# Optimization experiments

Measured on AMD Instinct MI355X. Metric: run time of the kernel, lower is better.

The kernel has to match this reference:

```python
import jax, jax.numpy as jnp
import numpy as np

B, T, I, H, O = 256, 512, 64, 512, 1


def _lstm_layer(x, Wih, Whh, bih, bhh):
    # x: [B, T, in]; Wih: [4H, in]; Whh: [4H, H]
    # Precompute input contribution for all timesteps (big GEMM, no recurrence).
    xg = jnp.einsum('bti,gi->btg', x, Wih) + bih + bhh  # [B, T, 4H]
    h0 = jnp.zeros((x.shape[0], Whh.shape[1]), x.dtype)
    c0 = jnp.zeros_like(h0)

    def step(carry, xt):
        h, c = carry
        gates = xt + h @ Whh.T  # [B, 4H]
        i, f, g, o = jnp.split(gates, 4, axis=-1)  # PyTorch gate order i,f,g,o
        i = jax.nn.sigmoid(i)
        f = jax.nn.sigmoid(f)
        g = jnp.tanh(g)
        o = jax.nn.sigmoid(o)
        c = f * c + i * g
        h = o * jnp.tanh(c)
        return (h, c), h

    _, hs = jax.lax.scan(step, (h0, c0), jnp.swapaxes(xg, 0, 1))  # [T, B, H]
    return jnp.swapaxes(hs, 0, 1)  # [B, T, H]


def setup_inputs() -> dict:
    key = jax.random.key(0)
    ks = jax.random.split(key, 12)
    s = 1.0 / np.sqrt(H)
    u = lambda k, shp: jax.random.uniform(k, shp, jnp.float32, -s, s)
    return {
        'x': jax.random.normal(ks[0], (B, T, I), jnp.float32),
        'Wih0': u(ks[1], (4 * H, I)),
        'Whh0': u(ks[2], (4 * H, H)),
        'bih0': u(ks[3], (4 * H,)),
        'bhh0': u(ks[4], (4 * H,)),
        'Wih1': u(ks[5], (4 * H, H)),
        'Whh1': u(ks[6], (4 * H, H)),
        'bih1': u(ks[7], (4 * H,)),
        'bhh1': u(ks[8], (4 * H,)),
        'Wfc': u(ks[9], (O, H)),
        'bfc': u(ks[10], (O,)),
    }


def reference(x, Wih0, Whh0, bih0, bhh0, Wih1, Whh1, bih1, bhh1, Wfc, bfc):
    h1 = _lstm_layer(x, Wih0, Whh0, bih0, bhh0)   # [B, T, H]
    h2 = _lstm_layer(h1, Wih1, Whh1, bih1, bhh1)  # [B, T, H]
    return h2[:, -1] @ Wfc.T + bfc  # [B, O]
```

## Files before the change

kernel.cpp:

```cpp
#include <hip/hip_runtime.h>

typedef unsigned short u16;
typedef unsigned long long u64;
typedef short bf16x8 __attribute__((ext_vector_type(8)));
typedef float f32x4 __attribute__((ext_vector_type(4)));

#define B_ 256
#define T_ 512
#define I_ 64
#define H_ 512
#define RING 32

#define OFF_F0    0u
#define OFF_F1    32768u
#define OFF_F2    65536u
#define OFF_F3    98304u
#define OFF_B0    131072u
#define OFF_B1    139264u
#define OFF_WIH0  147456u
#define OFF_WHH0  409600u
#define OFF_WIH1  2506752u
#define OFF_WHH1  4603904u
#define OFF_HX1   6701056u
#define OFF_H1R   7225344u
#define WS_NEEDED 15613952u

#define AQ __ATOMIC_RELAXED
#define SC __HIP_MEMORY_SCOPE_AGENT

static __device__ __forceinline__ u16 f2b(float f) {
  union { float f; unsigned u; } v; v.f = f;
  unsigned r = (v.u + 0x7FFFu + ((v.u >> 16) & 1u)) >> 16;
  return (u16)r;
}
static __device__ __forceinline__ float sigm(float x) { return 1.f / (1.f + __expf(-x)); }
static __device__ __forceinline__ float tanh_(float x) { return 1.f - 2.f / (__expf(2.f * x) + 1.f); }

static __device__ __forceinline__ void spin2(const unsigned* __restrict__ pa, unsigned tg) {
  unsigned a = __hip_atomic_load(pa, AQ, SC);
  for (;;) {
    unsigned b = __hip_atomic_load(pa, AQ, SC);
    if (!__any(a < tg)) break;
    a = __hip_atomic_load(pa, AQ, SC);
    if (!__any(b < tg)) break;
  }
}

__global__ void prep_kernel(const float* __restrict__ Wih0, const float* __restrict__ Whh0,
                            const float* __restrict__ bih0, const float* __restrict__ bhh0,
                            const float* __restrict__ Wih1, const float* __restrict__ Whh1,
                            const float* __restrict__ bih1, const float* __restrict__ bhh1,
                            const float* __restrict__ bfc, float* __restrict__ out,
                            char* __restrict__ ws) {
  unsigned* flags = (unsigned*)(ws + OFF_F0);
  float* b0 = (float*)(ws + OFF_B0);
  float* b1 = (float*)(ws + OFF_B1);
  u16* wih0b = (u16*)(ws + OFF_WIH0);
  u16* whh0b = (u16*)(ws + OFF_WHH0);
  u16* wih1b = (u16*)(ws + OFF_WIH1);
  u16* whh1b = (u16*)(ws + OFF_WHH1);

  long long i = (long long)blockIdx.x * 256 + threadIdx.x;
  if (i < 32768) { __hip_atomic_store(&flags[i], 0u, AQ, SC); return; }
  i -= 32768;
  if (i < 256) { out[i] = bfc[0]; return; }
  i -= 256;
  if (i < 2048) { b0[i] = bih0[i] + bhh0[i]; return; }
  i -= 2048;
  if (i < 2048) { b1[i] = bih1[i] + bhh1[i]; return; }
  i -= 2048;
  if (i < 131072) { wih0b[i] = f2b(Wih0[i]); return; }
  i -= 131072;
  if (i < 1048576) { whh0b[i] = f2b(Whh0[i]); return; }
  i -= 1048576;
  if (i < 1048576) { wih1b[i] = f2b(Wih1[i]); return; }
  i -= 1048576;
  if (i < 1048576) { whh1b[i] = f2b(Whh1[i]); return; }
}

template <bool IS_L0>
__device__ __forceinline__ void lstm_body(
    int ib, int jn,
    const float* __restrict__ x,
    const u16* __restrict__ Wib,
    const u16* __restrict__ Whb,
    const float* __restrict__ bias,
    unsigned* __restrict__ hx32,
    u16* __restrict__ h1ring,
    const float* __restrict__ Wfc, float* __restrict__ out,
    unsigned* __restrict__ fR,
    unsigned* __restrict__ fP,
    unsigned* __restrict__ fC,
    float* __restrict__ Gp_s)
{
  const int tid = threadIdx.x;
  const int wv = tid >> 6;
  const int lane = tid & 63;
  const int quad = lane >> 4;
  const int l15 = lane & 15;

  bf16x8 Bh[4][4];
#pragma unroll
  for (int r = 0; r < 4; ++r)
#pragma unroll
    for (int nt = 0; nt < 4; ++nt)
      Bh[r][nt] = *(const bf16x8*)&Whb[(size_t)(nt * 512 + jn * 16 + l15) * 512 +
                                       (wv * 4 + r) * 32 + quad * 8];
  bf16x8 Bx[4][4];
  bf16x8 Bx0[4];
  if constexpr (IS_L0) {
    if (wv < 2) {
#pragma unroll
      for (int nt = 0; nt < 4; ++nt)
        Bx0[nt] = *(const bf16x8*)&Wib[(size_t)(nt * 512 + jn * 16 + l15) * 64 +
                                       wv * 32 + quad * 8];
    }
  } else {
#pragma unroll
    for (int r = 0; r < 4; ++r)
#pragma unroll
      for (int nt = 0; nt < 4; ++nt)
        Bx[r][nt] = *(const bf16x8*)&Wib[(size_t)(nt * 512 + jn * 16 + l15) * 512 +
                                         (wv * 4 + r) * 32 + quad * 8];
  }

  const int erow = tid >> 3;
  const int ecp = tid & 7;
  float bias2[4][2];
#pragma unroll
  for (int g = 0; g < 4; ++g) {
    bias2[g][0] = bias[g * 512 + jn * 16 + 2 * ecp];
    bias2[g][1] = bias[g * 512 + jn * 16 + 2 * ecp + 1];
  }
  float cst2[2] = {0.f, 0.f};
  const f32x4 zf = {0.f, 0.f, 0.f, 0.f};
  const unsigned lineoff = ((unsigned)ib * 32 + jn) * 32;

  const int bg = ib * 32 + erow;
  const int hg = jn * 16 + 2 * ecp;
  const unsigned stoff = (unsigned)(((hg >> 3) * 256 + bg) * 4 + (ecp & 3));

  const unsigned* pollP;
  if constexpr (IS_L0)
    pollP = (lane < 32) ? &fR[lineoff + lane] : &fC[lineoff + (lane - 32)];
  else
    pollP = (lane < 32) ? &fR[lineoff + lane] : &fP[lineoff + (lane - 32)];

  if constexpr (!IS_L0) {
    if (wv == 0) spin2(&fP[lineoff + (lane & 31)], 1u);
    __syncthreads();
  }

  for (int t = 0; t < T_; ++t) {
    f32x4 acc[2][4];
#pragma unroll
    for (int mt = 0; mt < 2; ++mt)
#pragma unroll
      for (int nt = 0; nt < 4; ++nt) acc[mt][nt] = zf;

    if constexpr (IS_L0) {
      if (wv < 2) {
        const float* xp = x + ((size_t)(ib * 32 + l15) * T_ + t) * 64 + wv * 32 + quad * 8;
        const float* xq = xp + (size_t)16 * T_ * 64;
        float4 xa = *(const float4*)xp;
        float4 xb = *(const float4*)(xp + 4);
        float4 xc = *(const float4*)xq;
        float4 xd = *(const float4*)(xq + 4);
        union { unsigned u[4]; bf16x8 v; } P0, P1;
        P0.u[0] = (unsigned)f2b(xa.x) | ((unsigned)f2b(xa.y) << 16);
        P0.u[1] = (unsigned)f2b(xa.z) | ((unsigned)f2b(xa.w) << 16);
        P0.u[2] = (unsigned)f2b(xb.x) | ((unsigned)f2b(xb.y) << 16);
        P0.u[3] = (unsigned)f2b(xb.z) | ((unsigned)f2b(xb.w) << 16);
        P1.u[0] = (unsigned)f2b(xc.x) | ((unsigned)f2b(xc.y) << 16);
        P1.u[1] = (unsigned)f2b(xc.z) | ((unsigned)f2b(xc.w) << 16);
        P1.u[2] = (unsigned)f2b(xd.x) | ((unsigned)f2b(xd.y) << 16);
        P1.u[3] = (unsigned)f2b(xd.z) | ((unsigned)f2b(xd.w) << 16);
#pragma unroll
        for (int nt = 0; nt < 4; ++nt) {
          acc[0][nt] = __builtin_amdgcn_mfma_f32_16x16x32_bf16(P0.v, Bx0[nt], acc[0][nt], 0, 0, 0);
          acc[1][nt] = __builtin_amdgcn_mfma_f32_16x16x32_bf16(P1.v, Bx0[nt], acc[1][nt], 0, 0, 0);
        }
      }
      if (t && wv == 0) {
        const unsigned tg = (lane < 32) ? (unsigned)t
                            : ((t >= RING) ? (unsigned)(t - RING + 1) : 0u);
        spin2(pollP, tg);
      }
      __syncthreads();
    } else {
      const u64* hq1 = (const u64*)h1ring + (size_t)(t & (RING - 1)) * (B_ * H_ / 4);
#pragma unroll
      for (int r = 0; r < 4; ++r) {
        int ks = wv * 4 + r;
        bf16x8 af[2];
#pragma unroll
        for (int mt = 0; mt < 2; ++mt) {
          const u64* p = hq1 + (size_t)((ks * 4 + quad) * 256 + ib * 32 + mt * 16 + l15) * 2;
          union { u64 q[2]; bf16x8 v; } u;
          u.q[0] = __hip_atomic_load(p, AQ, SC);
          u.q[1] = __hip_atomic_load(p + 1, AQ, SC);
          af[mt] = u.v;
        }
#pragma unroll
        for (int nt = 0; nt < 4; ++nt) {
          acc[0][nt] = __builtin_amdgcn_mfma_f32_16x16x32_bf16(af[0], Bx[r][nt], acc[0][nt], 0, 0, 0);
          acc[1][nt] = __builtin_amdgcn_mfma_f32_16x16x32_bf16(af[1], Bx[r][nt], acc[1][nt], 0, 0, 0);
        }
      }
      if (wv == 0) {
        unsigned tP = (unsigned)(t + 2); if (tP > (unsigned)T_) tP = (unsigned)T_;
        const unsigned tg = (lane < 32) ? (unsigned)t : tP;
        spin2(pollP, tg);
      }
      __syncthreads();
    }

    __builtin_amdgcn_s_setprio(1);

    if (t) {
      const u64* hq;
      if constexpr (IS_L0)
        hq = (const u64*)h1ring + (size_t)((t - 1) & (RING - 1)) * (B_ * H_ / 4);
      else
        hq = (const u64*)hx32 + (size_t)(t & 1) * (B_ * H_ / 4);
      bf16x8 af[4][2];
#pragma unroll
      for (int r = 0; r < 4; ++r) {
        int ks = wv * 4 + r;
#pragma unroll
        for (int mt = 0; mt < 2; ++mt) {
          const u64* p = hq + (size_t)((ks * 4 + quad) * 256 + ib * 32 + mt * 16 + l15) * 2;
          union { u64 q[2]; bf16x8 v; } u;
          u.q[0] = __hip_atomic_load(p, AQ, SC);
          u.q[1] = __hip_atomic_load(p + 1, AQ, SC);
          af[r][mt] = u.v;
        }
      }
#pragma unroll
      for (int r = 0; r < 4; ++r)
#pragma unroll
        for (int mt = 0; mt < 2; ++mt)
#pragma unroll
          for (int nt = 0; nt < 4; ++nt)
            acc[mt][nt] = __builtin_amdgcn_mfma_f32_16x16x32_bf16(af[r][mt], Bh[r][nt],
                                                                  acc[mt][nt], 0, 0, 0);
    }

#pragma unroll
    for (int mt = 0; mt < 2; ++mt)
#pragma unroll
      for (int nt = 0; nt < 4; ++nt)
        *(f32x4*)&Gp_s[(nt * 16 + l15) * 132 + wv * 32 + mt * 16 + quad * 4] = acc[mt][nt];
    __syncthreads();

    {
      float pre[4][2];
#pragma unroll
      for (int g = 0; g < 4; ++g) {
#pragma unroll
        for (int j = 0; j < 2; ++j) {
          const int c = g * 16 + 2 * ecp + j;
          float s = bias2[g][j];
#pragma unroll
          for (int w = 0; w < 4; ++w) s += Gp_s[c * 132 + w * 32 + erow];
          pre[g][j] = s;
        }
      }
      float hv[2];
#pragma unroll
      for (int j = 0; j < 2; ++j) {
        float iv = sigm(pre[0][j]);
        float fv = sigm(pre[1][j]);
        float gv = tanh_(pre[2][j]);
        float ov = sigm(pre[3][j]);
        float cn = fv * cst2[j] + iv * gv;
        cst2[j] = cn;
        hv[j] = ov * tanh_(cn);
      }
      unsigned pack = (unsigned)f2b(hv[0]) | ((unsigned)f2b(hv[1]) << 16);
      if constexpr (IS_L0) {
        unsigned* ring32 = (unsigned*)h1ring;
        __hip_atomic_store(&ring32[(size_t)(t & (RING - 1)) * (B_ * H_ / 2) + stoff],
                           pack, AQ, SC);
      } else {
        __hip_atomic_store(&hx32[(size_t)((t + 1) & 1) * (B_ * H_ / 2) + stoff], pack, AQ, SC);
        if (t == T_ - 1) {
          float part = hv[0] * Wfc[hg] + hv[1] * Wfc[hg + 1];
          part += __shfl_down(part, 4, 8);
          part += __shfl_down(part, 2, 8);
          part += __shfl_down(part, 1, 8);
          if (ecp == 0) atomicAdd(&out[bg], part);
        }
      }
    }
    __builtin_amdgcn_s_setprio(0);

    __syncthreads();
    if (wv == 0) {
      unsigned val = (unsigned)(t + 1);
      if constexpr (IS_L0) {
        if (lane < 32)
          __hip_atomic_store(&fR[((unsigned)ib * 32 + lane) * 32 + jn], val, AQ, SC);
        else
          __hip_atomic_store(&fP[((unsigned)ib * 32 + (lane - 32)) * 32 + jn], val, AQ, SC);
      } else {
        if (lane < 32)
          __hip_atomic_store(&fR[((unsigned)ib * 32 + lane) * 32 + jn], val, AQ, SC);
        else
          __hip_atomic_store(&fC[((unsigned)ib * 32 + (lane - 32)) * 32 + jn], val, AQ, SC);
      }
    }
  }
}

__global__ __launch_bounds__(256, 2) void lstm_fused(
    const float* __restrict__ x,
    const u16* __restrict__ wih0, const u16* __restrict__ whh0, const float* __restrict__ b0,
    const u16* __restrict__ wih1, const u16* __restrict__ whh1, const float* __restrict__ b1,
    unsigned* __restrict__ hx1, u16* __restrict__ h1ring,
    const float* __restrict__ Wfc, float* __restrict__ out,
    unsigned* __restrict__ f0, unsigned* __restrict__ f1, unsigned* __restrict__ f2,
    unsigned* __restrict__ f3)
{
  __shared__ __align__(16) float Gp_s[64 * 132];
  const int bx = blockIdx.x;
  if (bx < 256)
    lstm_body<true>(bx & 7, bx >> 3, x, wih0, whh0, b0, (unsigned*)nullptr, h1ring,
                    (const float*)nullptr, (float*)nullptr, f0, f1, f3, Gp_s);
  else
    lstm_body<false>((bx - 256) & 7, (bx - 256) >> 3, (const float*)nullptr, wih1, whh1, b1,
                     hx1, h1ring, Wfc, out, f2, f1, f3, Gp_s);
}

extern "C" void kernel_launch(void* const* d_in, const int* in_sizes, int n_in,
                              void* d_out, int out_size, void* d_ws, size_t ws_size,
                              hipStream_t stream) {
  if (ws_size < (size_t)WS_NEEDED) return;

  const float* x    = (const float*)d_in[0];
  const float* Wih0 = (const float*)d_in[1];
  const float* Whh0 = (const float*)d_in[2];
  const float* bih0 = (const float*)d_in[3];
  const float* bhh0 = (const float*)d_in[4];
  const float* Wih1 = (const float*)d_in[5];
  const float* Whh1 = (const float*)d_in[6];
  const float* bih1 = (const float*)d_in[7];
  const float* bhh1 = (const float*)d_in[8];
  const float* Wfc  = (const float*)d_in[9];
  const float* bfc  = (const float*)d_in[10];

  char* ws = (char*)d_ws;
  unsigned* f0   = (unsigned*)(ws + OFF_F0);
  unsigned* f1   = (unsigned*)(ws + OFF_F1);
  unsigned* f2   = (unsigned*)(ws + OFF_F2);
  unsigned* f3   = (unsigned*)(ws + OFF_F3);
  float* b0      = (float*)(ws + OFF_B0);
  float* b1      = (float*)(ws + OFF_B1);
  u16* wih0b     = (u16*)(ws + OFF_WIH0);
  u16* whh0b     = (u16*)(ws + OFF_WHH0);
  u16* wih1b     = (u16*)(ws + OFF_WIH1);
  u16* whh1b     = (u16*)(ws + OFF_WHH1);
  unsigned* hx1  = (unsigned*)(ws + OFF_HX1);
  u16* h1ring    = (u16*)(ws + OFF_H1R);
  float* out     = (float*)d_out;

  prep_kernel<<<12948, 256, 0, stream>>>(Wih0, Whh0, bih0, bhh0, Wih1, Whh1, bih1, bhh1,
                                         bfc, out, ws);

  lstm_fused<<<512, 256, 0, stream>>>(x, wih0b, whh0b, b0, wih1b, whh1b, b1,
                                      hx1, h1ring, Wfc, out, f0, f1, f2, f3);
}
```

Measured before the change: 2.361 ms.

## Replace per-step block barrier with per-wave polling of needed flags

Each wave now spins only on the producer flags for the k-slices it reads (slot wv*8+lane&7), instead of wave 0 polling every flag and then releasing the block through __syncthreads. This removes the block-wide barrier from each timestep of the recurrence, so waves can start their MFMA work as soon as their own inputs are ready. A compiler memory fence is added after the spin. The cost is more atomic polling traffic, since every wave now spins, and correctness depends on each wave's flag subset covering all the data it reads.

```diff
diff --git a/kernel.cpp b/kernel.cpp
--- a/kernel.cpp
+++ b/kernel.cpp
@@ -44,6 +44,7 @@
     a = __hip_atomic_load(pa, AQ, SC);
     if (!__any(b < tg)) break;
   }
+  asm volatile("" ::: "memory");
 }
 
 __global__ void prep_kernel(const float* __restrict__ Wih0, const float* __restrict__ Whh0,
@@ -140,15 +141,17 @@
   const int hg = jn * 16 + 2 * ecp;
   const unsigned stoff = (unsigned)(((hg >> 3) * 256 + bg) * 4 + (ecp & 3));
 
-  const unsigned* pollP;
+  const int slot8 = wv * 8 + (lane & 7);
+  const unsigned* pollA;
+  const unsigned* pollB;
+  pollA = &fR[lineoff + slot8];
   if constexpr (IS_L0)
-    pollP = (lane < 32) ? &fR[lineoff + lane] : &fC[lineoff + (lane - 32)];
+    pollB = &fC[lineoff + (lane & 31)];
   else
-    pollP = (lane < 32) ? &fR[lineoff + lane] : &fP[lineoff + (lane - 32)];
+    pollB = &fP[lineoff + slot8];
 
   if constexpr (!IS_L0) {
-    if (wv == 0) spin2(&fP[lineoff + (lane & 31)], 1u);
-    __syncthreads();
+    spin2(pollB, 1u);
   }
 
   for (int t = 0; t < T_; ++t) {
@@ -181,12 +184,16 @@
           acc[1][nt] = __builtin_amdgcn_mfma_f32_16x16x32_bf16(P1.v, Bx0[nt], acc[1][nt], 0, 0, 0);
         }
       }
-      if (t && wv == 0) {
-        const unsigned tg = (lane < 32) ? (unsigned)t
-                            : ((t >= RING) ? (unsigned)(t - RING + 1) : 0u);
-        spin2(pollP, tg);
-      }
-      __syncthreads();
+      if (t) {
+        unsigned tg;
+        const unsigned* pp;
+        if (wv == 0 && lane >= 32) {
+          pp = pollB; tg = (t >= RING) ? (unsigned)(t - RING + 1) : 0u;
+        } else {
+          pp = pollA; tg = (unsigned)t;
+        }
+        spin2(pp, tg);
+      }
     } else {
       const u64* hq1 = (const u64*)h1ring + (size_t)(t & (RING - 1)) * (B_ * H_ / 4);
 #pragma unroll
@@ -207,12 +214,12 @@
           acc[1][nt] = __builtin_amdgcn_mfma_f32_16x16x32_bf16(af[1], Bx[r][nt], acc[1][nt], 0, 0, 0);
         }
       }
-      if (wv == 0) {
+      {
         unsigned tP = (unsigned)(t + 2); if (tP > (unsigned)T_) tP = (unsigned)T_;
         const unsigned tg = (lane < 32) ? (unsigned)t : tP;
-        spin2(pollP, tg);
-      }
-      __syncthreads();
+        const unsigned* pp = (lane < 32) ? pollA : pollB;
+        spin2(pp, tg);
+      }
     }
 
     __builtin_amdgcn_s_setprio(1);
```

Measured after the change: 3.155 ms. 33.6% more time.

## Merge pairs of LSTM blocks into 512-thread blocks to halve flag synchronization

Applied to the files above, without the earlier changes.

Each workgroup now has 512 threads and covers two adjacent 16-column hidden slices, so the grid shrinks from 512 to 256 blocks. The per-step flag polling and publishing fan-in per layer drops from 32 producers to 16. Shared memory for gate partials doubles, and a compiler memory barrier is added after the spin loop. The risk is lower occupancy (one block per CU) and larger __syncthreads cost with eight waves per barrier.

```diff
diff --git a/kernel.cpp b/kernel.cpp
--- a/kernel.cpp
+++ b/kernel.cpp
@@ -44,6 +44,7 @@
     a = __hip_atomic_load(pa, AQ, SC);
     if (!__any(b < tg)) break;
   }
+  asm volatile("" ::: "memory");
 }
 
 __global__ void prep_kernel(const float* __restrict__ Wih0, const float* __restrict__ Whh0,
@@ -94,17 +95,20 @@
     float* __restrict__ Gp_s)
 {
   const int tid = threadIdx.x;
-  const int wv = tid >> 6;
+  const int wgid = tid >> 6;
+  const int half = tid >> 8;
+  const int wv = wgid & 3;
   const int lane = tid & 63;
   const int quad = lane >> 4;
   const int l15 = lane & 15;
+  const int jne = jn * 2 + half;
 
   bf16x8 Bh[4][4];
 #pragma unroll
   for (int r = 0; r < 4; ++r)
 #pragma unroll
     for (int nt = 0; nt < 4; ++nt)
-      Bh[r][nt] = *(const bf16x8*)&Whb[(size_t)(nt * 512 + jn * 16 + l15) * 512 +
+      Bh[r][nt] = *(const bf16x8*)&Whb[(size_t)(nt * 512 + jne * 16 + l15) * 512 +
                                        (wv * 4 + r) * 32 + quad * 8];
   bf16x8 Bx[4][4];
   bf16x8 Bx0[4];
@@ -112,7 +116,7 @@
     if (wv < 2) {
 #pragma unroll
       for (int nt = 0; nt < 4; ++nt)
-        Bx0[nt] = *(const bf16x8*)&Wib[(size_t)(nt * 512 + jn * 16 + l15) * 64 +
+        Bx0[nt] = *(const bf16x8*)&Wib[(size_t)(nt * 512 + jne * 16 + l15) * 64 +
                                        wv * 32 + quad * 8];
     }
   } else {
@@ -120,36 +124,40 @@
     for (int r = 0; r < 4; ++r)
 #pragma unroll
       for (int nt = 0; nt < 4; ++nt)
-        Bx[r][nt] = *(const bf16x8*)&Wib[(size_t)(nt * 512 + jn * 16 + l15) * 512 +
+        Bx[r][nt] = *(const bf16x8*)&Wib[(size_t)(nt * 512 + jne * 16 + l15) * 512 +
                                          (wv * 4 + r) * 32 + quad * 8];
   }
 
-  const int erow = tid >> 3;
-  const int ecp = tid & 7;
+  const int htid = tid & 255;
+  const int erow = htid >> 3;
+  const int ecp = htid & 7;
   float bias2[4][2];
 #pragma unroll
   for (int g = 0; g < 4; ++g) {
-    bias2[g][0] = bias[g * 512 + jn * 16 + 2 * ecp];
-    bias2[g][1] = bias[g * 512 + jn * 16 + 2 * ecp + 1];
+    bias2[g][0] = bias[g * 512 + jne * 16 + 2 * ecp];
+    bias2[g][1] = bias[g * 512 + jne * 16 + 2 * ecp + 1];
   }
   float cst2[2] = {0.f, 0.f};
   const f32x4 zf = {0.f, 0.f, 0.f, 0.f};
-  const unsigned lineoff = ((unsigned)ib * 32 + jn) * 32;
+  const unsigned lineoff = ((unsigned)ib * 16 + jn) * 32;
 
   const int bg = ib * 32 + erow;
-  const int hg = jn * 16 + 2 * ecp;
+  const int hg = jne * 16 + 2 * ecp;
   const unsigned stoff = (unsigned)(((hg >> 3) * 256 + bg) * 4 + (ecp & 3));
 
-  const unsigned* pollP;
+  const unsigned* pollA = &fR[lineoff + (lane & 15)];
+  const unsigned* pollB;
   if constexpr (IS_L0)
-    pollP = (lane < 32) ? &fR[lineoff + lane] : &fC[lineoff + (lane - 32)];
+    pollB = &fC[lineoff + (lane & 15)];
   else
-    pollP = (lane < 32) ? &fR[lineoff + lane] : &fP[lineoff + (lane - 32)];
+    pollB = &fP[lineoff + (lane & 15)];
 
   if constexpr (!IS_L0) {
-    if (wv == 0) spin2(&fP[lineoff + (lane & 31)], 1u);
+    if (wgid == 0) spin2(pollB, 1u);
     __syncthreads();
   }
+
+  float* __restrict__ Gp = Gp_s + half * (64 * 132);
 
   for (int t = 0; t < T_; ++t) {
     f32x4 acc[2][4];
@@ -181,10 +189,10 @@
           acc[1][nt] = __builtin_amdgcn_mfma_f32_16x16x32_bf16(P1.v, Bx0[nt], acc[1][nt], 0, 0, 0);
         }
       }
-      if (t && wv == 0) {
+      if (t && wgid == 0) {
         const unsigned tg = (lane < 32) ? (unsigned)t
                             : ((t >= RING) ? (unsigned)(t - RING + 1) : 0u);
-        spin2(pollP, tg);
+        spin2((lane < 32) ? pollA : pollB, tg);
       }
       __syncthreads();
     } else {
@@ -207,10 +215,10 @@
           acc[1][nt] = __builtin_amdgcn_mfma_f32_16x16x32_bf16(af[1], Bx[r][nt], acc[1][nt], 0, 0, 0);
         }
       }
-      if (wv == 0) {
+      if (wgid == 0) {
         unsigned tP = (unsigned)(t + 2); if (tP > (unsigned)T_) tP = (unsigned)T_;
         const unsigned tg = (lane < 32) ? (unsigned)t : tP;
-        spin2(pollP, tg);
+        spin2((lane < 32) ? pollA : pollB, tg);
       }
       __syncthreads();
     }
@@ -250,7 +258,7 @@
     for (int mt = 0; mt < 2; ++mt)
 #pragma unroll
       for (int nt = 0; nt < 4; ++nt)
-        *(f32x4*)&Gp_s[(nt * 16 + l15) * 132 + wv * 32 + mt * 16 + quad * 4] = acc[mt][nt];
+        *(f32x4*)&Gp[(nt * 16 + l15) * 132 + wv * 32 + mt * 16 + quad * 4] = acc[mt][nt];
     __syncthreads();
 
     {
@@ -262,7 +270,7 @@
           const int c = g * 16 + 2 * ecp + j;
           float s = bias2[g][j];
 #pragma unroll
-          for (int w = 0; w < 4; ++w) s += Gp_s[c * 132 + w * 32 + erow];
+          for (int w = 0; w < 4; ++w) s += Gp[c * 132 + w * 32 + erow];
           pre[g][j] = s;
         }
       }
@@ -296,24 +304,24 @@
     __builtin_amdgcn_s_setprio(0);
 
     __syncthreads();
-    if (wv == 0) {
+    if (wgid == 0) {
       unsigned val = (unsigned)(t + 1);
       if constexpr (IS_L0) {
-        if (lane < 32)
-          __hip_atomic_store(&fR[((unsigned)ib * 32 + lane) * 32 + jn], val, AQ, SC);
-        else
-          __hip_atomic_store(&fP[((unsigned)ib * 32 + (lane - 32)) * 32 + jn], val, AQ, SC);
+        if (lane < 16)
+          __hip_atomic_store(&fR[((unsigned)ib * 16 + lane) * 32 + jn], val, AQ, SC);
+        else if (lane >= 32 && lane < 48)
+          __hip_atomic_store(&fP[((unsigned)ib * 16 + (lane - 32)) * 32 + jn], val, AQ, SC);
       } else {
-        if (lane < 32)
-          __hip_atomic_store(&fR[((unsigned)ib * 32 + lane) * 32 + jn], val, AQ, SC);
-        else
-          __hip_atomic_store(&fC[((unsigned)ib * 32 + (lane - 32)) * 32 + jn], val, AQ, SC);
-      }
-    }
-  }
-}
-
-__global__ __launch_bounds__(256, 2) void lstm_fused(
+        if (lane < 16)
+          __hip_atomic_store(&fR[((unsigned)ib * 16 + lane) * 32 + jn], val, AQ, SC);
+        else if (lane >= 32 && lane < 48)
+          __hip_atomic_store(&fC[((unsigned)ib * 16 + (lane - 32)) * 32 + jn], val, AQ, SC);
+      }
+    }
+  }
+}
+
+__global__ __launch_bounds__(512, 1) void lstm_fused(
     const float* __restrict__ x,
     const u16* __restrict__ wih0, const u16* __restrict__ whh0, const float* __restrict__ b0,
     const u16* __restrict__ wih1, const u16* __restrict__ whh1, const float* __restrict__ b1,
@@ -322,13 +330,13 @@
     unsigned* __restrict__ f0, unsigned* __restrict__ f1, unsigned* __restrict__ f2,
     unsigned* __restrict__ f3)
 {
-  __shared__ __align__(16) float Gp_s[64 * 132];
+  __shared__ __align__(16) float Gp_s[2 * 64 * 132];
   const int bx = blockIdx.x;
-  if (bx < 256)
+  if (bx < 128)
     lstm_body<true>(bx & 7, bx >> 3, x, wih0, whh0, b0, (unsigned*)nullptr, h1ring,
                     (const float*)nullptr, (float*)nullptr, f0, f1, f3, Gp_s);
   else
-    lstm_body<false>((bx - 256) & 7, (bx - 256) >> 3, (const float*)nullptr, wih1, whh1, b1,
+    lstm_body<false>((bx - 128) & 7, (bx - 128) >> 3, (const float*)nullptr, wih1, whh1, b1,
                      hx1, h1ring, Wfc, out, f2, f1, f3, Gp_s);
 }
 
@@ -367,6 +375,6 @@
   prep_kernel<<<12948, 256, 0, stream>>>(Wih0, Whh0, bih0, bhh0, Wih1, Whh1, bih1, bhh1,
                                          bfc, out, ws);
 
-  lstm_fused<<<512, 256, 0, stream>>>(x, wih0b, whh0b, b0, wih1b, whh1b, b1,
+  lstm_fused<<<256, 512, 0, stream>>>(x, wih0b, whh0b, b0, wih1b, whh1b, b1,
                                       hx1, h1ring, Wfc, out, f0, f1, f2, f3);
 }
```

After: 2.706 ms. +14.6%, slower.

## Halve grid so each block processes two batch tiles with XCD-aware mapping

Applied to the files above, without the earlier changes.

Each persistent block now handles two batch tiles (ib and ib+4) in alternating phases per timestep, so the grid shrinks from 512 to 256 blocks while reusing the register-resident weights for both tiles. Block-to-(batch,hidden) mapping is rearranged so blocks sharing a batch group sit on the same XCD pair, which should localise flag and hidden-state traffic. Per-step work per block doubles and the two phases run serially, trading parallelism for fewer co-resident blocks and less cross-die synchronisation.

```diff
diff --git a/kernel.cpp b/kernel.cpp
--- a/kernel.cpp
+++ b/kernel.cpp
@@ -44,6 +44,7 @@
     a = __hip_atomic_load(pa, AQ, SC);
     if (!__any(b < tg)) break;
   }
+  asm volatile("" ::: "memory");
 }
 
 __global__ void prep_kernel(const float* __restrict__ Wih0, const float* __restrict__ Whh0,
@@ -79,8 +80,192 @@
 }
 
 template <bool IS_L0>
+__device__ __forceinline__ void phase(
+    int t, int ib, int jn,
+    const float* __restrict__ x,
+    const bf16x8 (&Bh)[4][4], const bf16x8 (&Bx)[4][4], const bf16x8 (&Bx0)[4],
+    const float (&bias2)[4][2], float (&cst2)[2],
+    unsigned* __restrict__ hx32, u16* __restrict__ h1ring,
+    const float* __restrict__ Wfc, float* __restrict__ out,
+    unsigned* __restrict__ fR, unsigned* __restrict__ fP, unsigned* __restrict__ fC,
+    float* __restrict__ Gp_s,
+    const unsigned* __restrict__ pollA, const unsigned* __restrict__ pollB)
+{
+  const int tid = threadIdx.x;
+  const int wv = tid >> 6;
+  const int lane = tid & 63;
+  const int quad = lane >> 4;
+  const int l15 = lane & 15;
+  const int erow = tid >> 3;
+  const int ecp = tid & 7;
+  const int bg = ib * 32 + erow;
+  const int hg = jn * 16 + 2 * ecp;
+  const unsigned stoff = (unsigned)(((hg >> 3) * 256 + bg) * 4 + (ecp & 3));
+  const f32x4 zf = {0.f, 0.f, 0.f, 0.f};
+
+  f32x4 acc[2][4];
+#pragma unroll
+  for (int mt = 0; mt < 2; ++mt)
+#pragma unroll
+    for (int nt = 0; nt < 4; ++nt) acc[mt][nt] = zf;
+
+  if constexpr (IS_L0) {
+    if (wv < 2) {
+      const float* xp = x + ((size_t)(ib * 32 + l15) * T_ + t) * 64 + wv * 32 + quad * 8;
+      const float* xq = xp + (size_t)16 * T_ * 64;
+      float4 xa = *(const float4*)xp;
+      float4 xb = *(const float4*)(xp + 4);
+      float4 xc = *(const float4*)xq;
+      float4 xd = *(const float4*)(xq + 4);
+      union { unsigned u[4]; bf16x8 v; } P0, P1;
+      P0.u[0] = (unsigned)f2b(xa.x) | ((unsigned)f2b(xa.y) << 16);
+      P0.u[1] = (unsigned)f2b(xa.z) | ((unsigned)f2b(xa.w) << 16);
+      P0.u[2] = (unsigned)f2b(xb.x) | ((unsigned)f2b(xb.y) << 16);
+      P0.u[3] = (unsigned)f2b(xb.z) | ((unsigned)f2b(xb.w) << 16);
+      P1.u[0] = (unsigned)f2b(xc.x) | ((unsigned)f2b(xc.y) << 16);
+      P1.u[1] = (unsigned)f2b(xc.z) | ((unsigned)f2b(xc.w) << 16);
+      P1.u[2] = (unsigned)f2b(xd.x) | ((unsigned)f2b(xd.y) << 16);
+      P1.u[3] = (unsigned)f2b(xd.z) | ((unsigned)f2b(xd.w) << 16);
+#pragma unroll
+      for (int nt = 0; nt < 4; ++nt) {
+        acc[0][nt] = __builtin_amdgcn_mfma_f32_16x16x32_bf16(P0.v, Bx0[nt], acc[0][nt], 0, 0, 0);
+        acc[1][nt] = __builtin_amdgcn_mfma_f32_16x16x32_bf16(P1.v, Bx0[nt], acc[1][nt], 0, 0, 0);
+      }
+    }
+    if (t && wv == 0) {
+      const unsigned tg = (lane < 32) ? (unsigned)t
+                          : ((t >= RING) ? (unsigned)(t - RING + 1) : 0u);
+      spin2((lane < 32) ? pollA : pollB, tg);
+    }
+    __syncthreads();
+  } else {
+    const u64* hq1 = (const u64*)h1ring + (size_t)(t & (RING - 1)) * (B_ * H_ / 4);
+#pragma unroll
+    for (int r = 0; r < 4; ++r) {
+      int ks = wv * 4 + r;
+      bf16x8 af[2];
+#pragma unroll
+      for (int mt = 0; mt < 2; ++mt) {
+        const u64* p = hq1 + (size_t)((ks * 4 + quad) * 256 + ib * 32 + mt * 16 + l15) * 2;
+        union { u64 q[2]; bf16x8 v; } u;
+        u.q[0] = __hip_atomic_load(p, AQ, SC);
+        u.q[1] = __hip_atomic_load(p + 1, AQ, SC);
+        af[mt] = u.v;
+      }
+#pragma unroll
+      for (int nt = 0; nt < 4; ++nt) {
+        acc[0][nt] = __builtin_amdgcn_mfma_f32_16x16x32_bf16(af[0], Bx[r][nt], acc[0][nt], 0, 0, 0);
+        acc[1][nt] = __builtin_amdgcn_mfma_f32_16x16x32_bf16(af[1], Bx[r][nt], acc[1][nt], 0, 0, 0);
+      }
+    }
+    if (wv == 0) {
+      unsigned tP = (unsigned)(t + 2); if (tP > (unsigned)T_) tP = (unsigned)T_;
+      const unsigned tg = (lane < 32) ? (unsigned)t : tP;
+      spin2((lane < 32) ? pollA : pollB, tg);
+    }
+    __syncthreads();
+  }
+
+  __builtin_amdgcn_s_setprio(1);
+
+  if (t) {
+    const u64* hq;
+    if constexpr (IS_L0)
+      hq = (const u64*)h1ring + (size_t)((t - 1) & (RING - 1)) * (B_ * H_ / 4);
+    else
+      hq = (const u64*)hx32 + (size_t)(t & 1) * (B_ * H_ / 4);
+    bf16x8 af[4][2];
+#pragma unroll
+    for (int r = 0; r < 4; ++r) {
+      int ks = wv * 4 + r;
+#pragma unroll
+      for (int mt = 0; mt < 2; ++mt) {
+        const u64* p = hq + (size_t)((ks * 4 + quad) * 256 + ib * 32 + mt * 16 + l15) * 2;
+        union { u64 q[2]; bf16x8 v; } u;
+        u.q[0] = __hip_atomic_load(p, AQ, SC);
+        u.q[1] = __hip_atomic_load(p + 1, AQ, SC);
+        af[r][mt] = u.v;
+      }
+    }
+#pragma unroll
+    for (int r = 0; r < 4; ++r)
+#pragma unroll
+      for (int mt = 0; mt < 2; ++mt)
+#pragma unroll
+        for (int nt = 0; nt < 4; ++nt)
+          acc[mt][nt] = __builtin_amdgcn_mfma_f32_16x16x32_bf16(af[r][mt], Bh[r][nt],
+                                                                acc[mt][nt], 0, 0, 0);
+  }
+
+#pragma unroll
+  for (int mt = 0; mt < 2; ++mt)
+#pragma unroll
+    for (int nt = 0; nt < 4; ++nt)
+      *(f32x4*)&Gp_s[(nt * 16 + l15) * 132 + wv * 32 + mt * 16 + quad * 4] = acc[mt][nt];
+  __syncthreads();
+
+  {
+    float pre[4][2];
+#pragma unroll
+    for (int g = 0; g < 4; ++g) {
+#pragma unroll
+      for (int j = 0; j < 2; ++j) {
+        const int c = g * 16 + 2 * ecp + j;
+        float s = bias2[g][j];
+#pragma unroll
+        for (int w = 0; w < 4; ++w) s += Gp_s[c * 132 + w * 32 + erow];
+        pre[g][j] = s;
+      }
+    }
+    float hv[2];
+#pragma unroll
+    for (int j = 0; j < 2; ++j) {
+      float iv = sigm(pre[0][j]);
+      float fv = sigm(pre[1][j]);
+      float gv = tanh_(pre[2][j]);
+      float ov = sigm(pre[3][j]);
+      float cn = fv * cst2[j] + iv * gv;
+      cst2[j] = cn;
+      hv[j] = ov * tanh_(cn);
+    }
+    unsigned pack = (unsigned)f2b(hv[0]) | ((unsigned)f2b(hv[1]) << 16);
+    if constexpr (IS_L0) {
+      unsigned* ring32 = (unsigned*)h1ring;
+      __hip_atomic_store(&ring32[(size_t)(t & (RING - 1)) * (B_ * H_ / 2) + stoff],
+                         pack, AQ, SC);
+    } else {
+      __hip_atomic_store(&hx32[(size_t)((t + 1) & 1) * (B_ * H_ / 2) + stoff], pack, AQ, SC);
+      if (t == T_ - 1) {
+        float part = hv[0] * Wfc[hg] + hv[1] * Wfc[hg + 1];
+        part += __shfl_down(part, 4, 8);
+        part += __shfl_down(part, 2, 8);
+        part += __shfl_down(part, 1, 8);
+        if (ecp == 0) atomicAdd(&out[bg], part);
+      }
+    }
+  }
+  __builtin_amdgcn_s_setprio(0);
+
+  __syncthreads();
+  if (wv == 0) {
+    unsigned val = (unsigned)(t + 1);
+    if constexpr (IS_L0) {
+      if (lane < 32)
+        __hip_atomic_store(&fR[((unsigned)ib * 32 + lane) * 32 + jn], val, AQ, SC);
+      else
+        __hip_atomic_store(&fP[((unsigned)ib * 32 + (lane - 32)) * 32 + jn], val, AQ, SC);
+    } else {
+      if (lane < 32)
+        __hip_atomic_store(&fR[((unsigned)ib * 32 + lane) * 32 + jn], val, AQ, SC);
+      else
+        __hip_atomic_store(&fC[((unsigned)ib * 32 + (lane - 32)) * 32 + jn], val, AQ, SC);
+    }
+  }
+}
+
+template <bool IS_L0>
 __device__ __forceinline__ void lstm_body(
-    int ib, int jn,
+    int ibA, int jn,
     const float* __restrict__ x,
     const u16* __restrict__ Wib,
     const u16* __restrict__ Whb,
@@ -98,6 +283,7 @@
   const int lane = tid & 63;
   const int quad = lane >> 4;
   const int l15 = lane & 15;
+  const int ibB = ibA + 4;
 
   bf16x8 Bh[4][4];
 #pragma unroll
@@ -124,7 +310,6 @@
                                          (wv * 4 + r) * 32 + quad * 8];
   }
 
-  const int erow = tid >> 3;
   const int ecp = tid & 7;
   float bias2[4][2];
 #pragma unroll
@@ -132,184 +317,33 @@
     bias2[g][0] = bias[g * 512 + jn * 16 + 2 * ecp];
     bias2[g][1] = bias[g * 512 + jn * 16 + 2 * ecp + 1];
   }
-  float cst2[2] = {0.f, 0.f};
-  const f32x4 zf = {0.f, 0.f, 0.f, 0.f};
-  const unsigned lineoff = ((unsigned)ib * 32 + jn) * 32;
-
-  const int bg = ib * 32 + erow;
-  const int hg = jn * 16 + 2 * ecp;
-  const unsigned stoff = (unsigned)(((hg >> 3) * 256 + bg) * 4 + (ecp & 3));
-
-  const unsigned* pollP;
-  if constexpr (IS_L0)
-    pollP = (lane < 32) ? &fR[lineoff + lane] : &fC[lineoff + (lane - 32)];
-  else
-    pollP = (lane < 32) ? &fR[lineoff + lane] : &fP[lineoff + (lane - 32)];
+  float cstA[2] = {0.f, 0.f};
+  float cstB[2] = {0.f, 0.f};
+
+  const unsigned loA = ((unsigned)ibA * 32 + jn) * 32;
+  const unsigned loB = ((unsigned)ibB * 32 + jn) * 32;
+  const unsigned* pollA_A = &fR[loA + (lane & 31)];
+  const unsigned* pollA_B = &fR[loB + (lane & 31)];
+  const unsigned* pollB_A;
+  const unsigned* pollB_B;
+  if constexpr (IS_L0) {
+    pollB_A = &fC[loA + (lane & 31)];
+    pollB_B = &fC[loB + (lane & 31)];
+  } else {
+    pollB_A = &fP[loA + (lane & 31)];
+    pollB_B = &fP[loB + (lane & 31)];
+  }
 
   if constexpr (!IS_L0) {
-    if (wv == 0) spin2(&fP[lineoff + (lane & 31)], 1u);
+    if (wv == 0) { spin2(pollB_A, 1u); spin2(pollB_B, 1u); }
     __syncthreads();
   }
 
   for (int t = 0; t < T_; ++t) {
-    f32x4 acc[2][4];
-#pragma unroll
-    for (int mt = 0; mt < 2; ++mt)
-#pragma unroll
-      for (int nt = 0; nt < 4; ++nt) acc[mt][nt] = zf;
-
-    if constexpr (IS_L0) {
-      if (wv < 2) {
-        const float* xp = x + ((size_t)(ib * 32 + l15) * T_ + t) * 64 + wv * 32 + quad * 8;
-        const float* xq = xp + (size_t)16 * T_ * 64;
-        float4 xa = *(const float4*)xp;
-        float4 xb = *(const float4*)(xp + 4);
-        float4 xc = *(const float4*)xq;
-        float4 xd = *(const float4*)(xq + 4);
-        union { unsigned u[4]; bf16x8 v; } P0, P1;
-        P0.u[0] = (unsigned)f2b(xa.x) | ((unsigned)f2b(xa.y) << 16);
-        P0.u[1] = (unsigned)f2b(xa.z) | ((unsigned)f2b(xa.w) << 16);
-        P0.u[2] = (unsigned)f2b(xb.x) | ((unsigned)f2b(xb.y) << 16);
-        P0.u[3] = (unsigned)f2b(xb.z) | ((unsigned)f2b(xb.w) << 16);
-        P1.u[0] = (unsigned)f2b(xc.x) | ((unsigned)f2b(xc.y) << 16);
-        P1.u[1] = (unsigned)f2b(xc.z) | ((unsigned)f2b(xc.w) << 16);
-        P1.u[2] = (unsigned)f2b(xd.x) | ((unsigned)f2b(xd.y) << 16);
-        P1.u[3] = (unsigned)f2b(xd.z) | ((unsigned)f2b(xd.w) << 16);
-#pragma unroll
-        for (int nt = 0; nt < 4; ++nt) {
-          acc[0][nt] = __builtin_amdgcn_mfma_f32_16x16x32_bf16(P0.v, Bx0[nt], acc[0][nt], 0, 0, 0);
-          acc[1][nt] = __builtin_amdgcn_mfma_f32_16x16x32_bf16(P1.v, Bx0[nt], acc[1][nt], 0, 0, 0);
-        }
-      }
-      if (t && wv == 0) {
-        const unsigned tg = (lane < 32) ? (unsigned)t
-                            : ((t >= RING) ? (unsigned)(t - RING + 1) : 0u);
-        spin2(pollP, tg);
-      }
-      __syncthreads();
-    } else {
-      const u64* hq1 = (const u64*)h1ring + (size_t)(t & (RING - 1)) * (B_ * H_ / 4);
-#pragma unroll
-      for (int r = 0; r < 4; ++r) {
-        int ks = wv * 4 + r;
-        bf16x8 af[2];
-#pragma unroll
-        for (int mt = 0; mt < 2; ++mt) {
-          const u64* p = hq1 + (size_t)((ks * 4 + quad) * 256 + ib * 32 + mt * 16 + l15) * 2;
-          union { u64 q[2]; bf16x8 v; } u;
-          u.q[0] = __hip_atomic_load(p, AQ, SC);
-          u.q[1] = __hip_atomic_load(p + 1, AQ, SC);
-          af[mt] = u.v;
-        }
-#pragma unroll
-        for (int nt = 0; nt < 4; ++nt) {
-          acc[0][nt] = __builtin_amdgcn_mfma_f32_16x16x32_bf16(af[0], Bx[r][nt], acc[0][nt], 0, 0, 0);
-          acc[1][nt] = __builtin_amdgcn_mfma_f32_16x16x32_bf16(af[1], Bx[r][nt], acc[1][nt], 0, 0, 0);
-        }
-      }
-      if (wv == 0) {
-        unsigned tP = (unsigned)(t + 2); if (tP > (unsigned)T_) tP = (unsigned)T_;
-        const unsigned tg = (lane < 32) ? (unsigned)t : tP;
-        spin2(pollP, tg);
-      }
-      __syncthreads();
-    }
-
-    __builtin_amdgcn_s_setprio(1);
-
-    if (t) {
-      const u64* hq;
-      if constexpr (IS_L0)
-        hq = (const u64*)h1ring + (size_t)((t - 1) & (RING - 1)) * (B_ * H_ / 4);
-      else
-        hq = (const u64*)hx32 + (size_t)(t & 1) * (B_ * H_ / 4);
-      bf16x8 af[4][2];
-#pragma unroll
-      for (int r = 0; r < 4; ++r) {
-        int ks = wv * 4 + r;
-#pragma unroll
-        for (int mt = 0; mt < 2; ++mt) {
-          const u64* p = hq + (size_t)((ks * 4 + quad) * 256 + ib * 32 + mt * 16 + l15) * 2;
-          union { u64 q[2]; bf16x8 v; } u;
-          u.q[0] = __hip_atomic_load(p, AQ, SC);
-          u.q[1] = __hip_atomic_load(p + 1, AQ, SC);
-          af[r][mt] = u.v;
-        }
-      }
-#pragma unroll
-      for (int r = 0; r < 4; ++r)
-#pragma unroll
-        for (int mt = 0; mt < 2; ++mt)
-#pragma unroll
-          for (int nt = 0; nt < 4; ++nt)
-            acc[mt][nt] = __builtin_amdgcn_mfma_f32_16x16x32_bf16(af[r][mt], Bh[r][nt],
-                                                                  acc[mt][nt], 0, 0, 0);
-    }
-
-#pragma unroll
-    for (int mt = 0; mt < 2; ++mt)
-#pragma unroll
-      for (int nt = 0; nt < 4; ++nt)
-        *(f32x4*)&Gp_s[(nt * 16 + l15) * 132 + wv * 32 + mt * 16 + quad * 4] = acc[mt][nt];
-    __syncthreads();
-
-    {
-      float pre[4][2];
-#pragma unroll
-      for (int g = 0; g < 4; ++g) {
-#pragma unroll
-        for (int j = 0; j < 2; ++j) {
-          const int c = g * 16 + 2 * ecp + j;
-          float s = bias2[g][j];
-#pragma unroll
-          for (int w = 0; w < 4; ++w) s += Gp_s[c * 132 + w * 32 + erow];
-          pre[g][j] = s;
-        }
-      }
-      float hv[2];
-#pragma unroll
-      for (int j = 0; j < 2; ++j) {
-        float iv = sigm(pre[0][j]);
-        float fv = sigm(pre[1][j]);
-        float gv = tanh_(pre[2][j]);
-        float ov = sigm(pre[3][j]);
-        float cn = fv * cst2[j] + iv * gv;
-        cst2[j] = cn;
-        hv[j] = ov * tanh_(cn);
-      }
-      unsigned pack = (unsigned)f2b(hv[0]) | ((unsigned)f2b(hv[1]) << 16);
-      if constexpr (IS_L0) {
-        unsigned* ring32 = (unsigned*)h1ring;
-        __hip_atomic_store(&ring32[(size_t)(t & (RING - 1)) * (B_ * H_ / 2) + stoff],
-                           pack, AQ, SC);
-      } else {
-        __hip_atomic_store(&hx32[(size_t)((t + 1) & 1) * (B_ * H_ / 2) + stoff], pack, AQ, SC);
-        if (t == T_ - 1) {
-          float part = hv[0] * Wfc[hg] + hv[1] * Wfc[hg + 1];
-          part += __shfl_down(part, 4, 8);
-          part += __shfl_down(part, 2, 8);
-          part += __shfl_down(part, 1, 8);
-          if (ecp == 0) atomicAdd(&out[bg], part);
-        }
-      }
-    }
-    __builtin_amdgcn_s_setprio(0);
-
-    __syncthreads();
-    if (wv == 0) {
-      unsigned val = (unsigned)(t + 1);
-      if constexpr (IS_L0) {
-        if (lane < 32)
-          __hip_atomic_store(&fR[((unsigned)ib * 32 + lane) * 32 + jn], val, AQ, SC);
-        else
-          __hip_atomic_store(&fP[((unsigned)ib * 32 + (lane - 32)) * 32 + jn], val, AQ, SC);
-      } else {
-        if (lane < 32)
-          __hip_atomic_store(&fR[((unsigned)ib * 32 + lane) * 32 + jn], val, AQ, SC);
-        else
-          __hip_atomic_store(&fC[((unsigned)ib * 32 + (lane - 32)) * 32 + jn], val, AQ, SC);
-      }
-    }
+    phase<IS_L0>(t, ibA, jn, x, Bh, Bx, Bx0, bias2, cstA, hx32, h1ring, Wfc, out,
+                 fR, fP, fC, Gp_s, pollA_A, pollB_A);
+    phase<IS_L0>(t, ibB, jn, x, Bh, Bx, Bx0, bias2, cstB, hx32, h1ring, Wfc, out,
+                 fR, fP, fC, Gp_s, pollA_B, pollB_B);
   }
 }
 
@@ -324,12 +358,17 @@
 {
   __shared__ __align__(16) float Gp_s[64 * 132];
   const int bx = blockIdx.x;
-  if (bx < 256)
-    lstm_body<true>(bx & 7, bx >> 3, x, wih0, whh0, b0, (unsigned*)nullptr, h1ring,
+  const int v = (bx < 128) ? bx : bx - 128;
+  const int xcd = v & 7;
+  const int r = v >> 3;
+  const int P = xcd >> 1;
+  const int jn = (xcd & 1) * 16 + r;
+  if (bx < 128)
+    lstm_body<true>(P, jn, x, wih0, whh0, b0, (unsigned*)nullptr, h1ring,
                     (const float*)nullptr, (float*)nullptr, f0, f1, f3, Gp_s);
   else
-    lstm_body<false>((bx - 256) & 7, (bx - 256) >> 3, (const float*)nullptr, wih1, whh1, b1,
-                     hx1, h1ring, Wfc, out, f2, f1, f3, Gp_s);
+    lstm_body<false>(P, jn, (const float*)nullptr, wih1, whh1, b1, hx1, h1ring,
+                     Wfc, out, f2, f1, f3, Gp_s);
 }
 
 extern "C" void kernel_launch(void* const* d_in, const int* in_sizes, int n_in,
@@ -367,6 +406,6 @@
   prep_kernel<<<12948, 256, 0, stream>>>(Wih0, Whh0, bih0, bhh0, Wih1, Whh1, bih1, bhh1,
                                          bfc, out, ws);
 
-  lstm_fused<<<512, 256, 0, stream>>>(x, wih0b, whh0b, b0, wih1b, whh1b, b1,
+  lstm_fused<<<256, 256, 0, stream>>>(x, wih0b, whh0b, b0, wih1b, whh1b, b1,
                                       hx1, h1ring, Wfc, out, f0, f1, f2, f3);
 }
```

Result: slower. 3.784 ms (+60.3%).
